# Kernel optimization log

Hardware: AMD Instinct MI355X
Metric: run time of the kernel (lower is better)

## Reference

```python
import jax, jax.numpy as jnp
import numpy as np

IN_DIM = 512
OUT_DIM = 512
KEY_DIM = 512
FILTER_LENGTH = 32
STRIDE = 4
B, T = 8, 2048


def setup_inputs() -> dict:
    key = jax.random.key(0)
    ks = jax.random.split(key, 7)
    s_in = 1.0 / np.sqrt(IN_DIM)
    x = jax.random.normal(ks[0], (B, T, IN_DIM), dtype=jnp.float32)
    Wq = jax.random.uniform(ks[1], (IN_DIM, KEY_DIM), jnp.float32, -s_in, s_in)
    bq = jax.random.uniform(ks[2], (KEY_DIM,), jnp.float32, -s_in, s_in)
    Wk = jax.random.uniform(ks[3], (IN_DIM, KEY_DIM), jnp.float32, -s_in, s_in)
    bk = jax.random.uniform(ks[4], (KEY_DIM,), jnp.float32, -s_in, s_in)
    Wv = jax.random.uniform(ks[5], (IN_DIM, OUT_DIM), jnp.float32, -s_in, s_in)
    bv = jax.random.uniform(ks[6], (OUT_DIM,), jnp.float32, -s_in, s_in)
    return {"x": x, "Wq": Wq, "bq": bq, "Wk": Wk, "bk": bk, "Wv": Wv, "bv": bv}


def reference(x, Wq, bq, Wk, bk, Wv, bv):
    # x: (B, T, in_dim)
    Bsz, T_, _ = x.shape
    F = FILTER_LENGTH
    T_out = (T_ - F) // STRIDE + 1
    starts = jnp.arange(T_out) * STRIDE                 # (T_out,)
    win_idx = starts[:, None] + jnp.arange(F)[None, :]  # (T_out, F)
    center_idx = starts + F // 2                        # (T_out,)

    q = x @ Wq + bq   # (B, T, key_dim)
    k = x @ Wk + bk   # (B, T, key_dim)
    v = x @ Wv + bv   # (B, T, out_dim)

    q_c = q[:, center_idx]    # (B, T_out, key_dim) query at window center
    k_w = k[:, win_idx]       # (B, T_out, F, key_dim)
    v_w = v[:, win_idx]       # (B, T_out, F, out_dim)

    scale = 1.0 / jnp.sqrt(jnp.asarray(KEY_DIM, dtype=q.dtype))
    scores = jnp.einsum('btd,btfd->btf', q_c, k_w) * scale  # (B, T_out, F)
    attn = jax.nn.softmax(scores, axis=-1)
    out = jnp.einsum('btf,btfd->btd', attn, v_w)            # (B, T_out, out_dim)
    return out
```

## Files before the change

### kernel.cpp

```cpp
#include <hip/hip_runtime.h>
#include <hip/hip_bf16.h>
#include <cstdint>

#define FLT 32
#define TOUT 505
#define TT 2048
#define MROWS 16384
#define QROWS 4040
#define KDIM 512
#define BK 64
#define NT 8

typedef float f32x4 __attribute__((ext_vector_type(4)));
typedef __bf16 bf16x8 __attribute__((ext_vector_type(8)));

static __device__ __forceinline__ ushort f2bf(float f) {
  uint32_t u = __float_as_uint(f);
  uint32_t r = (u + 0x7fffu + ((u >> 16) & 1u)) >> 16;
  return (ushort)r;
}
static __device__ __forceinline__ float bf2f(ushort h) {
  return __uint_as_float(((uint32_t)h) << 16);
}
static __device__ __forceinline__ void pack8(const float4& lo, const float4& hi, ushort* v8) {
  v8[0] = f2bf(lo.x); v8[1] = f2bf(lo.y); v8[2] = f2bf(lo.z); v8[3] = f2bf(lo.w);
  v8[4] = f2bf(hi.x); v8[5] = f2bf(hi.y); v8[6] = f2bf(hi.z); v8[7] = f2bf(hi.w);
}

__global__ void wprep_kernel(const float* __restrict__ Wq, const float* __restrict__ Wk,
                             const float* __restrict__ Wv, const float* __restrict__ bq,
                             const float* __restrict__ bk, const float* __restrict__ bv,
                             ushort* __restrict__ wt, float* __restrict__ bias) {
  const int bid = blockIdx.x;
  const int tid = threadIdx.x;
  if (bid < 192) {
    __shared__ ushort lds[64][66];
    int mat = bid >> 6;
    int w = bid & 63;
    int k0 = (w >> 3) * 64, n0 = (w & 7) * 64;
    const float* W = (mat == 0) ? Wq : (mat == 1) ? Wk : Wv;
    int nn = tid & 63;
    #pragma unroll
    for (int r = 0; r < 16; ++r) {
      int kk = r * 4 + (tid >> 6);
      lds[kk][nn] = f2bf(W[(size_t)(k0 + kk) * 512 + n0 + nn]);
    }
    __syncthreads();
    int kk2 = tid & 63;
    #pragma unroll
    for (int r = 0; r < 16; ++r) {
      int nn2 = r * 4 + (tid >> 6);
      wt[(size_t)(mat * 512 + n0 + nn2) * 512 + k0 + kk2] = lds[kk2][nn2];
    }
  } else {
    #pragma unroll
    for (int e = 0; e < 6; ++e) {
      int n = tid * 6 + e;
      const float* bsrc = (n < 512) ? bq : (n < 1024) ? bk : bv;
      bias[n] = bsrc[n & 511];
    }
  }
}

__global__ __launch_bounds__(256, 2) void gemm_kernel(
    const float* __restrict__ xf, const ushort* __restrict__ wt,
    const float* __restrict__ bias, ushort* __restrict__ kv, ushort* __restrict__ qc) {
  __shared__ char smem[33792];
  ushort* const As = (ushort*)smem;
  ushort* const Bs = (ushort*)(smem + 16384);

  const int tid = threadIdx.x;
  const int lane = tid & 63;
  const int wv = tid >> 6;
  const int bid = blockIdx.x;

  int m0, n0, ost, gather, mlim;
  const ushort* wtb;
  const float* biasb;
  ushort* outp;
  if (bid >= 128) {
    int l = bid - 128;
    int swz = (l & 7) * 128 + (l >> 3);
    m0 = (swz >> 3) * 128; n0 = (swz & 7) * 128;
    wtb = wt + (size_t)512 * KDIM; biasb = bias + 512;
    outp = kv; ost = 1024; gather = 0; mlim = MROWS;
  } else {
    int swz = (bid & 7) * 16 + (bid >> 3);
    m0 = (swz >> 2) * 128; n0 = (swz & 3) * 128;
    wtb = wt; biasb = bias;
    outp = qc; ost = 512; gather = 1; mlim = QROWS;
  }

  const float* aF[4];
  uint aDst[4];
  const ushort* bS[4];
  #pragma unroll
  for (int i = 0; i < 4; ++i) {
    int idx = i * 4096 + tid * 16;
    int row = idx >> 7;
    int colb = idx & 127;
    aDst[i] = (uint)(row * 128 + (colb ^ ((row & 7) << 4)));
    int scol = (colb ^ ((row & 7) << 4)) >> 1;
    size_t arow;
    if (gather) {
      int r = m0 + row;
      if (r > QROWS - 1) r = QROWS - 1;
      int bb = r / TOUT;
      int t2 = r - bb * TOUT;
      arow = (size_t)bb * TT + (size_t)t2 * 4 + FLT / 2;
    } else {
      arow = (size_t)(m0 + row);
    }
    aF[i] = xf + arow * KDIM + (colb >> 1);
    bS[i] = wtb + (size_t)(n0 + row) * KDIM + scol;
  }

  const int fr = lane & 15;
  const int fq = lane >> 4;
  const int wr = wv >> 1;
  const int wc = wv & 1;

  f32x4 acc[4][4];
  #pragma unroll
  for (int i = 0; i < 4; ++i)
    #pragma unroll
    for (int j = 0; j < 4; ++j) acc[i][j] = (f32x4){0.f, 0.f, 0.f, 0.f};

  float4 aLo[4], aHi[4];
  #pragma unroll
  for (int i = 0; i < 4; ++i) {
    aLo[i] = *reinterpret_cast<const float4*>(aF[i]);
    aHi[i] = *reinterpret_cast<const float4*>(aF[i] + 4);
  }

  for (int t = 0; t < NT; ++t) {
    __syncthreads();
    const int koff = t * BK;
    #pragma unroll
    for (int i = 0; i < 4; ++i) {
      __builtin_amdgcn_global_load_lds(
          (const __attribute__((address_space(1))) unsigned int*)(bS[i] + koff),
          (__attribute__((address_space(3))) unsigned int*)((char*)Bs + i * 4096 + tid * 16),
          16, 0, 0);
    }
    #pragma unroll
    for (int i = 0; i < 4; ++i) {
      ushort v8[8]; pack8(aLo[i], aHi[i], v8);
      *reinterpret_cast<uint4*>((char*)As + aDst[i]) = *reinterpret_cast<const uint4*>(v8);
    }
    __syncthreads();

    if (t < NT - 1) {
      #pragma unroll
      for (int i = 0; i < 4; ++i) {
        aLo[i] = *reinterpret_cast<const float4*>(aF[i] + koff + BK);
        aHi[i] = *reinterpret_cast<const float4*>(aF[i] + koff + BK + 4);
      }
    }

    #pragma unroll
    for (int ks = 0; ks < 2; ++ks) {
      bf16x8 af[4], bg[4];
      #pragma unroll
      for (int i = 0; i < 4; ++i) {
        int ra = wr * 64 + i * 16 + fr;
        int ca = ks * 64 + fq * 16;
        af[i] = *reinterpret_cast<const bf16x8*>(
            (const char*)As + ra * 128 + (ca ^ ((ra & 7) << 4)));
        int rb = wc * 64 + i * 16 + fr;
        bg[i] = *reinterpret_cast<const bf16x8*>(
            (const char*)Bs + rb * 128 + (ca ^ ((rb & 7) << 4)));
      }
      #pragma unroll
      for (int i = 0; i < 4; ++i)
        #pragma unroll
        for (int j = 0; j < 4; ++j)
          acc[i][j] = __builtin_amdgcn_mfma_f32_16x16x32_bf16(af[i], bg[j], acc[i][j], 0, 0, 0);
    }
  }

  __syncthreads();
  ushort* const ep = (ushort*)smem;
  #pragma unroll
  for (int j = 0; j < 4; ++j) {
    int colg = n0 + wc * 64 + j * 16 + fr;
    int coll = wc * 64 + j * 16 + fr;
    float bvl = biasb[colg];
    #pragma unroll
    for (int i = 0; i < 4; ++i) {
      int rowl = wr * 64 + i * 16 + fq * 4;
      #pragma unroll
      for (int r = 0; r < 4; ++r)
        ep[(rowl + r) * 132 + coll] = f2bf(acc[i][j][r] + bvl);
    }
  }
  __syncthreads();
  #pragma unroll
  for (int it = 0; it < 8; ++it) {
    int row = it * 16 + (tid >> 4);
    int gr = m0 + row;
    if (gr < mlim) {
      uint4 val = *reinterpret_cast<const uint4*>(&ep[row * 132 + (tid & 15) * 8]);
      *reinterpret_cast<uint4*>(outp + (size_t)gr * ost + n0 + (tid & 15) * 8) = val;
    }
  }
}

__global__ __launch_bounds__(256) void attn_kernel(
    const ushort* __restrict__ kv,
    const ushort* __restrict__ qc,
    float* __restrict__ out) {
  __shared__ float q_lds[KDIM];
  __shared__ float s_lds[FLT];
  __shared__ float p_lds[FLT];

  const int bid = blockIdx.x;
  const int b = bid & 7;
  const int t = bid >> 3;
  const size_t base_row = (size_t)b * TT + (size_t)t * 4;
  const int tid = threadIdx.x;
  const int lane = tid & 63;
  const int wv = tid >> 6;

  {
    const ushort* qrow = qc + ((size_t)b * TOUT + t) * KDIM;
    uint v = *reinterpret_cast<const uint*>(qrow + tid * 2);
    q_lds[tid * 2]     = bf2f((ushort)(v & 0xffffu));
    q_lds[tid * 2 + 1] = bf2f((ushort)(v >> 16));
  }
  __syncthreads();

  const int fl = lane >> 3;
  const int f = wv * 8 + fl;
  const int sub = lane & 7;
  const ushort* krow = kv + (base_row + f) * 1024;
  float acc = 0.f;
  #pragma unroll
  for (int j = 0; j < 8; ++j) {
    int d = (j * 8 + sub) * 8;
    uint4 kv4 = *reinterpret_cast<const uint4*>(krow + d);
    const ushort* ks = reinterpret_cast<const ushort*>(&kv4);
    #pragma unroll
    for (int e = 0; e < 8; ++e) acc += q_lds[d + e] * bf2f(ks[e]);
  }
  acc += __shfl_xor(acc, 1);
  acc += __shfl_xor(acc, 2);
  acc += __shfl_xor(acc, 4);
  if (sub == 0) s_lds[f] = acc * 0.04419417382415922f;
  __syncthreads();

  float m = -1e30f;
  #pragma unroll
  for (int i = 0; i < FLT; ++i) m = fmaxf(m, s_lds[i]);
  if (tid < FLT) p_lds[tid] = __expf(s_lds[tid] - m);
  __syncthreads();
  float sum = 0.f;
  #pragma unroll
  for (int i = 0; i < FLT; ++i) sum += p_lds[i];
  const float inv = 1.f / sum;

  const int d = tid * 2;
  float o0 = 0.f, o1 = 0.f;
  const ushort* vbase = kv + base_row * 1024 + 512 + d;
  #pragma unroll
  for (int ff = 0; ff < FLT; ++ff) {
    uint vvv = *reinterpret_cast<const uint*>(vbase + (size_t)ff * 1024);
    float w = p_lds[ff] * inv;
    o0 += w * bf2f((ushort)(vvv & 0xffffu));
    o1 += w * bf2f((ushort)(vvv >> 16));
  }
  float2* op = reinterpret_cast<float2*>(out + ((size_t)b * TOUT + t) * 512 + d);
  *op = make_float2(o0, o1);
}

extern "C" void kernel_launch(void* const* d_in, const int* in_sizes, int n_in,
                              void* d_out, int out_size, void* d_ws, size_t ws_size,
                              hipStream_t stream) {
  const float* x  = (const float*)d_in[0];
  const float* Wq = (const float*)d_in[1];
  const float* bq = (const float*)d_in[2];
  const float* Wk = (const float*)d_in[3];
  const float* bk = (const float*)d_in[4];
  const float* Wv = (const float*)d_in[5];
  const float* bv = (const float*)d_in[6];
  float* out = (float*)d_out;

  char* ws = (char*)d_ws;
  ushort* wt   = (ushort*)ws;
  float*  bias = (float*)(ws + 1572864);
  ushort* kvb  = (ushort*)(ws + 1581056);
  ushort* qc   = (ushort*)(ws + 1581056 + 33554432);

  hipLaunchKernelGGL(wprep_kernel, dim3(193), dim3(256), 0, stream,
                     Wq, Wk, Wv, bq, bk, bv, wt, bias);
  hipLaunchKernelGGL(gemm_kernel, dim3(1152), dim3(256), 0, stream,
                     x, wt, bias, kvb, qc);
  hipLaunchKernelGGL(attn_kernel, dim3(QROWS), dim3(256), 0, stream, kvb, qc, out);
}
```

Baseline: 73.90 us.

## Double-buffer GEMM LDS tiles with manual waitcnt barriers and MFMA priority

The GEMM main loop now ping-pongs between two LDS buffers (64KB dynamic shared memory), so the next tile's global-to-LDS loads and A packing can overlap the MFMA work on the current tile. The compiler's __syncthreads is replaced by explicit s_waitcnt and s_barrier, and s_setprio is raised around the MFMA block. Block ordering is also swapped so the larger K/V tiles are scheduled before the gathered Q tiles. The doubled LDS footprint may reduce how many blocks fit per CU, and the hand-written waitcnt counts must stay correct for the loads to be safe.

```diff
diff --git a/kernel.cpp b/kernel.cpp
--- a/kernel.cpp
+++ b/kernel.cpp
@@ -65,9 +65,7 @@
 __global__ __launch_bounds__(256, 2) void gemm_kernel(
     const float* __restrict__ xf, const ushort* __restrict__ wt,
     const float* __restrict__ bias, ushort* __restrict__ kv, ushort* __restrict__ qc) {
-  __shared__ char smem[33792];
-  ushort* const As = (ushort*)smem;
-  ushort* const Bs = (ushort*)(smem + 16384);
+  extern __shared__ char smem[];
 
   const int tid = threadIdx.x;
   const int lane = tid & 63;
@@ -78,14 +76,14 @@
   const ushort* wtb;
   const float* biasb;
   ushort* outp;
-  if (bid >= 128) {
-    int l = bid - 128;
-    int swz = (l & 7) * 128 + (l >> 3);
+  if (bid < 1024) {
+    int swz = (bid & 7) * 128 + (bid >> 3);
     m0 = (swz >> 3) * 128; n0 = (swz & 7) * 128;
     wtb = wt + (size_t)512 * KDIM; biasb = bias + 512;
     outp = kv; ost = 1024; gather = 0; mlim = MROWS;
   } else {
-    int swz = (bid & 7) * 16 + (bid >> 3);
+    int b2 = bid - 1024;
+    int swz = (b2 & 7) * 16 + (b2 >> 3);
     m0 = (swz >> 2) * 128; n0 = (swz & 3) * 128;
     wtb = wt; biasb = bias;
     outp = qc; ost = 512; gather = 1; mlim = QROWS;
@@ -132,32 +130,55 @@
     aLo[i] = *reinterpret_cast<const float4*>(aF[i]);
     aHi[i] = *reinterpret_cast<const float4*>(aF[i] + 4);
   }
+  asm volatile("" ::: "memory");
+  #pragma unroll
+  for (int i = 0; i < 4; ++i) {
+    __builtin_amdgcn_global_load_lds(
+        (const __attribute__((address_space(1))) unsigned int*)bS[i],
+        (__attribute__((address_space(3))) unsigned int*)(smem + 32768 + i * 4096 + tid * 16),
+        16, 0, 0);
+  }
+  asm volatile("s_waitcnt vmcnt(4)" ::: "memory");
+  #pragma unroll
+  for (int i = 0; i < 4; ++i) {
+    ushort v8[8]; pack8(aLo[i], aHi[i], v8);
+    *reinterpret_cast<uint4*>(smem + aDst[i]) = *reinterpret_cast<const uint4*>(v8);
+  }
 
   for (int t = 0; t < NT; ++t) {
-    __syncthreads();
-    const int koff = t * BK;
-    #pragma unroll
-    for (int i = 0; i < 4; ++i) {
-      __builtin_amdgcn_global_load_lds(
-          (const __attribute__((address_space(1))) unsigned int*)(bS[i] + koff),
-          (__attribute__((address_space(3))) unsigned int*)((char*)Bs + i * 4096 + tid * 16),
-          16, 0, 0);
-    }
-    #pragma unroll
-    for (int i = 0; i < 4; ++i) {
-      ushort v8[8]; pack8(aLo[i], aHi[i], v8);
-      *reinterpret_cast<uint4*>((char*)As + aDst[i]) = *reinterpret_cast<const uint4*>(v8);
-    }
-    __syncthreads();
-
+    const int cur = t & 1;
+    char* const Ac = smem + cur * 16384;
+    char* const Bc = smem + 32768 + cur * 16384;
     if (t < NT - 1) {
+      const int koff = (t + 1) * BK;
+      char* const An = smem + (cur ^ 1) * 16384;
+      char* const Bn = smem + 32768 + (cur ^ 1) * 16384;
       #pragma unroll
       for (int i = 0; i < 4; ++i) {
-        aLo[i] = *reinterpret_cast<const float4*>(aF[i] + koff + BK);
-        aHi[i] = *reinterpret_cast<const float4*>(aF[i] + koff + BK + 4);
+        aLo[i] = *reinterpret_cast<const float4*>(aF[i] + koff);
+        aHi[i] = *reinterpret_cast<const float4*>(aF[i] + koff + 4);
       }
-    }
-
+      asm volatile("" ::: "memory");
+      #pragma unroll
+      for (int i = 0; i < 4; ++i) {
+        __builtin_amdgcn_global_load_lds(
+            (const __attribute__((address_space(1))) unsigned int*)(bS[i] + koff),
+            (__attribute__((address_space(3))) unsigned int*)(Bn + i * 4096 + tid * 16),
+            16, 0, 0);
+      }
+      asm volatile("s_waitcnt vmcnt(4)" ::: "memory");
+      #pragma unroll
+      for (int i = 0; i < 4; ++i) {
+        ushort v8[8]; pack8(aLo[i], aHi[i], v8);
+        *reinterpret_cast<uint4*>(An + aDst[i]) = *reinterpret_cast<const uint4*>(v8);
+      }
+    } else {
+      asm volatile("s_waitcnt vmcnt(0)" ::: "memory");
+    }
+    asm volatile("s_waitcnt lgkmcnt(0)" ::: "memory");
+    __builtin_amdgcn_s_barrier();
+
+    __builtin_amdgcn_s_setprio(1);
     #pragma unroll
     for (int ks = 0; ks < 2; ++ks) {
       bf16x8 af[4], bg[4];
@@ -165,11 +186,9 @@
       for (int i = 0; i < 4; ++i) {
         int ra = wr * 64 + i * 16 + fr;
         int ca = ks * 64 + fq * 16;
-        af[i] = *reinterpret_cast<const bf16x8*>(
-            (const char*)As + ra * 128 + (ca ^ ((ra & 7) << 4)));
+        af[i] = *reinterpret_cast<const bf16x8*>(Ac + ra * 128 + (ca ^ ((ra & 7) << 4)));
         int rb = wc * 64 + i * 16 + fr;
-        bg[i] = *reinterpret_cast<const bf16x8*>(
-            (const char*)Bs + rb * 128 + (ca ^ ((rb & 7) << 4)));
+        bg[i] = *reinterpret_cast<const bf16x8*>(Bc + rb * 128 + (ca ^ ((rb & 7) << 4)));
       }
       #pragma unroll
       for (int i = 0; i < 4; ++i)
@@ -177,6 +196,9 @@
         for (int j = 0; j < 4; ++j)
           acc[i][j] = __builtin_amdgcn_mfma_f32_16x16x32_bf16(af[i], bg[j], acc[i][j], 0, 0, 0);
     }
+    __builtin_amdgcn_s_setprio(0);
+    asm volatile("" ::: "memory");
+    __builtin_amdgcn_s_barrier();
   }
 
   __syncthreads();
@@ -291,9 +313,12 @@
   ushort* kvb  = (ushort*)(ws + 1581056);
   ushort* qc   = (ushort*)(ws + 1581056 + 33554432);
 
+  hipFuncSetAttribute((const void*)gemm_kernel,
+                      hipFuncAttributeMaxDynamicSharedMemorySize, 65536);
+
   hipLaunchKernelGGL(wprep_kernel, dim3(193), dim3(256), 0, stream,
                      Wq, Wk, Wv, bq, bk, bv, wt, bias);
-  hipLaunchKernelGGL(gemm_kernel, dim3(1152), dim3(256), 0, stream,
+  hipLaunchKernelGGL(gemm_kernel, dim3(1152), dim3(256), 65536, stream,
                      x, wt, bias, kvb, qc);
   hipLaunchKernelGGL(attn_kernel, dim3(QROWS), dim3(256), 0, stream, kvb, qc, out);
 }
```

After: 73.76 us. About the same (-0.2%).
